# Optimization experiments

Hardware: AMD Instinct MI355X
Metric: run time of the kernel (lower is better)

Reference implementation:

```python
import jax, jax.numpy as jnp
import numpy as np

D_MODEL = 1024
NHEAD = 16
D_K = D_MODEL // NHEAD
MAX_REL = 1024


def setup_inputs() -> dict:
    key = jax.random.key(0)
    ks = jax.random.split(key, 6)
    B, S = 4, 2048
    s = 1.0 / np.sqrt(D_MODEL)
    x = jax.random.normal(ks[0], (B, S, D_MODEL), dtype=jnp.float32)
    W_qkv = jax.random.normal(ks[1], (D_MODEL, 3 * D_MODEL), dtype=jnp.float32) * s
    b_qkv = jnp.zeros((3 * D_MODEL,), dtype=jnp.float32)
    W_out = jax.random.normal(ks[2], (D_MODEL, D_MODEL), dtype=jnp.float32) * s
    b_out = jnp.zeros((D_MODEL,), dtype=jnp.float32)
    # torch init is zeros; use small random so bias path is exercised
    rel_bias = jax.random.normal(ks[3], (2 * MAX_REL + 1, NHEAD), dtype=jnp.float32) * 0.02
    return {"x": x, "W_qkv": W_qkv, "b_qkv": b_qkv, "W_out": W_out,
            "b_out": b_out, "rel_bias": rel_bias}


def reference(x, W_qkv, b_qkv, W_out, b_out, rel_bias):
    B, S, D = x.shape
    qkv = x @ W_qkv + b_qkv                      # [B,S,3D]
    qkv = qkv.reshape(B, S, 3, NHEAD, D_K)
    q, k, v = qkv[:, :, 0], qkv[:, :, 1], qkv[:, :, 2]  # [B,S,H,dk]
    # scores: [B,H,S,S]
    scores = jnp.einsum('bihd,bjhd->bhij', q, k) / jnp.sqrt(jnp.float32(D_K))
    idxs = jnp.arange(S)
    rel = jnp.clip(idxs[:, None] - idxs[None, :] + MAX_REL, 0, 2 * MAX_REL)  # [S,S]
    bias = rel_bias[rel]                         # [S,S,H]
    scores = scores + jnp.transpose(bias, (2, 0, 1))[None]  # broadcast over batch
    attn = jax.nn.softmax(scores, axis=-1)       # dropout p=0 (eval)
    out = jnp.einsum('bhij,bjhd->bihd', attn, v).reshape(B, S, D)
    return out @ W_out + b_out
```

## Files before the change

### kernel.cpp

```cpp
#include <hip/hip_runtime.h>

#define S_LEN 2048
#define NHEADS 16
#define DK 64
#define DMODEL 1024
#define QSCALE 0.18033688011f

typedef float f32x4 __attribute__((ext_vector_type(4)));
typedef _Float16 f16x8 __attribute__((ext_vector_type(8)));
typedef _Float16 f16x4 __attribute__((ext_vector_type(4)));
typedef __fp16 h16x2 __attribute__((ext_vector_type(2)));

__device__ __forceinline__ unsigned short f2h_bits(float f) {
  _Float16 h = (_Float16)f;
  unsigned short u; __builtin_memcpy(&u, &h, 2); return u;
}

__device__ __forceinline__ f32x4 mfma16(f16x8 a, f16x8 b, f32x4 c) {
  return __builtin_amdgcn_mfma_f32_16x16x32_f16(a, b, c, 0, 0, 0);
}
__device__ __forceinline__ f32x4 mfma16k16(f16x4 a, f16x4 b, f32x4 c) {
  return __builtin_amdgcn_mfma_f32_16x16x16f16(a, b, c, 0, 0, 0);
}
__device__ __forceinline__ f16x8 frag_ld(const unsigned short* p) {
  return *(const f16x8*)p;
}

#define GLD_LDS(g, l)                                                          \
  __builtin_amdgcn_global_load_lds(                                            \
      (const __attribute__((address_space(1))) void*)(g),                      \
      (__attribute__((address_space(3))) void*)(l), 16, 0, 0)

__global__ void convert_f32_f16(const float* __restrict__ in,
                                unsigned short* __restrict__ out, int n4) {
  int i = blockIdx.x * blockDim.x + threadIdx.x;
  if (i < n4) {
    f32x4 v = *(const f32x4*)(in + (size_t)i * 4);
    unsigned short o[4];
#pragma unroll
    for (int j = 0; j < 4; j++) o[j] = f2h_bits(v[j]);
    *(uint2*)(out + (size_t)i * 4) = *(const uint2*)o;
  }
}

__global__ void transpose_f32_f16(const float* __restrict__ in,
                                  unsigned short* __restrict__ out, int R, int C) {
  __shared__ unsigned short tile[32][33];
  int bx = blockIdx.x * 32, by = blockIdx.y * 32;
  int tx = threadIdx.x, ty = threadIdx.y;
  for (int i = ty; i < 32; i += 8)
    tile[i][tx] = f2h_bits(in[(size_t)(by + i) * C + bx + tx]);
  __syncthreads();
  for (int i = ty; i < 32; i += 8)
    out[(size_t)(bx + i) * R + by + tx] = tile[tx][i];
}

__launch_bounds__(256)
__global__ void gemm_bt(const unsigned short* __restrict__ A,
                        const unsigned short* __restrict__ Bt,
                        int M, int N, int K, int mode,
                        const float* __restrict__ bias,
                        float* __restrict__ out0,
                        unsigned short* __restrict__ q_o,
                        unsigned short* __restrict__ k_o,
                        unsigned short* __restrict__ v_o) {
  __shared__ __attribute__((aligned(16))) unsigned short As[128 * 32];
  __shared__ __attribute__((aligned(16))) unsigned short Bs[128 * 32];
  const int tid = threadIdx.x;
  const int w = tid >> 6, lane = tid & 63;
  const int wm = w >> 1, wn = w & 1;
  const int col = lane & 15, quad = lane >> 4;
  const int m0 = blockIdx.y * 128, n0 = blockIdx.x * 128;
  const f32x4 fzero = {0.f, 0.f, 0.f, 0.f};
  f32x4 acc[4][4];
#pragma unroll
  for (int i = 0; i < 4; i++)
#pragma unroll
    for (int j = 0; j < 4; j++) acc[i][j] = fzero;

  for (int k0 = 0; k0 < K; k0 += 32) {
    __syncthreads();
#pragma unroll
    for (int it = 0; it < 2; it++) {
      int c = it * 256 + tid;
      GLD_LDS(A + (size_t)(m0 + (c >> 2)) * K + k0 + (c & 3) * 8, &As[c * 8]);
      GLD_LDS(Bt + (size_t)(n0 + (c >> 2)) * K + k0 + (c & 3) * 8, &Bs[c * 8]);
    }
    __syncthreads();
    f16x8 af[4], bfr[4];
#pragma unroll
    for (int mi = 0; mi < 4; mi++)
      af[mi] = frag_ld(&As[(wm * 64 + mi * 16 + col) * 32 + quad * 8]);
#pragma unroll
    for (int ni = 0; ni < 4; ni++)
      bfr[ni] = frag_ld(&Bs[(wn * 64 + ni * 16 + col) * 32 + quad * 8]);
#pragma unroll
    for (int mi = 0; mi < 4; mi++)
#pragma unroll
      for (int ni = 0; ni < 4; ni++)
        acc[mi][ni] = mfma16(af[mi], bfr[ni], acc[mi][ni]);
  }

#pragma unroll
  for (int mi = 0; mi < 4; mi++) {
#pragma unroll
    for (int ni = 0; ni < 4; ni++) {
      int gm_b = m0 + wm * 64 + mi * 16 + quad * 4;
      int gn = n0 + wn * 64 + ni * 16 + col;
      float bv = bias[gn];
      if (mode == 1) {
#pragma unroll
        for (int r = 0; r < 4; r++)
          out0[(size_t)(gm_b + r) * N + gn] = acc[mi][ni][r] + bv;
      } else {
        int b = gm_b >> 11, s0 = gm_b & 2047;
        int t = gn >> 10, hd = gn & 1023;
        int h = hd >> 6, d = hd & 63;
        size_t bh = (size_t)(b * NHEADS + h);
        if (t == 2) {
          unsigned short o4[4];
#pragma unroll
          for (int r = 0; r < 4; r++) o4[r] = f2h_bits(acc[mi][ni][r] + bv);
          *(uint2*)&v_o[(bh * DK + d) * S_LEN + s0] = *(const uint2*)o4;
        } else {
          unsigned short* dst = (t == 0) ? q_o : k_o;
          float sc = (t == 0) ? QSCALE : 1.0f;
#pragma unroll
          for (int r = 0; r < 4; r++)
            dst[(bh * S_LEN + s0 + r) * DK + d] = f2h_bits((acc[mi][ni][r] + bv) * sc);
        }
      }
    }
  }
}

__launch_bounds__(256, 3)
__global__ void attn_kernel(const unsigned short* __restrict__ Q,
                            const unsigned short* __restrict__ K,
                            const unsigned short* __restrict__ Vt,
                            const float* __restrict__ rel_bias,
                            unsigned short* __restrict__ ctx) {
  __shared__ __attribute__((aligned(16))) char smem[25088];
  unsigned short* Ks = (unsigned short*)smem;
  unsigned short* Vs = (unsigned short*)(smem + 8192);
  float* brev = (float*)(smem + 16384);
  float* lred = (float*)(smem + 24832);
  float* red  = (float*)smem;

  const int tid = threadIdx.x;
  const int w = tid >> 6, lane = tid & 63;
  const int col = lane & 15, quad = lane >> 4;
  const int c7 = col & 7;
  const int bid = blockIdx.x;
  const int xcd = bid & 7, slot = bid >> 3;
  const int bh = (slot >> 5) * 8 + xcd;
  const int qt = slot & 31;
  const int h = bh & (NHEADS - 1), b = bh >> 4;
  const unsigned short* qp = Q + (size_t)bh * S_LEN * DK;
  const unsigned short* kp = K + (size_t)bh * S_LEN * DK;
  const unsigned short* vp = Vt + (size_t)bh * DK * S_LEN;
  const f32x4 fzero = {0.f, 0.f, 0.f, 0.f};

  const int tbase = 1985 - qt * 64;
#pragma unroll
  for (int it = 0; it < 9; it++) {
    int idx = it * 256 + tid;
    if (idx < 2112) {
      int rel = 3072 - (tbase + idx);
      rel = rel < 0 ? 0 : (rel > 2048 ? 2048 : rel);
      brev[idx] = rel_bias[rel * NHEADS + h] * 1.44269504089f;
    }
  }

  f16x8 qb[4][2];
#pragma unroll
  for (int qs = 0; qs < 4; qs++)
#pragma unroll
    for (int ks = 0; ks < 2; ks++)
      qb[qs][ks] = frag_ld(qp + (size_t)(qt * 64 + qs * 16 + col) * DK + ks * 32 + quad * 8);

  const int cA = tid, cB = 256 + tid;
  const int rA = cA >> 3, gA = (cA & 7) ^ (rA & 7);
  const int rB = cB >> 3, gB = (cB & 7) ^ (rB & 7);
  const unsigned short* kgA = kp + rA * DK + gA * 8;
  const unsigned short* kgB = kp + rB * DK + gB * 8;
  const unsigned short* vgA = vp + (size_t)rA * S_LEN + gA * 8;
  const unsigned short* vgB = vp + (size_t)rB * S_LEN + gB * 8;
  unsigned short* lkA = &Ks[cA * 8];
  unsigned short* lkB = &Ks[cB * 8];
  unsigned short* lvA = &Vs[cA * 8];
  unsigned short* lvB = &Vs[cB * 8];

  const float* bp = &brev[w * 16 + quad * 4 - col + 15];

  f32x4 o[4][4];
  float rsum[4];
#pragma unroll
  for (int qs = 0; qs < 4; qs++) {
#pragma unroll
    for (int ds = 0; ds < 4; ds++) o[qs][ds] = fzero;
    rsum[qs] = 0.f;
  }

  const int kaoff0 = (w * 16 + col) * 64 + (quad ^ c7) * 8;
  const int kaoff1 = (w * 16 + col) * 64 + ((4 + quad) ^ c7) * 8;
  const int vgrp = ((w * 2 + (quad >> 1)) ^ c7) * 8 + (quad & 1) * 4;

  for (int ck = 0; ck < S_LEN / 64; ck++) {
    __syncthreads();
    GLD_LDS(kgA, lkA); GLD_LDS(kgB, lkB);
    GLD_LDS(vgA, lvA); GLD_LDS(vgB, lvB);
    __syncthreads();

    f16x8 ka0 = frag_ld(&Ks[kaoff0]);
    f16x8 ka1 = frag_ld(&Ks[kaoff1]);
    f16x4 vb[4];
#pragma unroll
    for (int ds = 0; ds < 4; ds++)
      vb[ds] = *(const f16x4*)&Vs[(ds * 16 + col) * 64 + vgrp];

#pragma unroll
    for (int qs = 0; qs < 4; qs++) {
      f32x4 bias4;
#pragma unroll
      for (int r = 0; r < 4; r++) bias4[r] = bp[(3 - qs) * 16 + r];
      f32x4 sc = mfma16(ka1, qb[qs][1], mfma16(ka0, qb[qs][0], bias4));
      float p0 = __builtin_amdgcn_exp2f(sc[0]);
      float p1 = __builtin_amdgcn_exp2f(sc[1]);
      float p2 = __builtin_amdgcn_exp2f(sc[2]);
      float p3 = __builtin_amdgcn_exp2f(sc[3]);
      rsum[qs] += (p0 + p1) + (p2 + p3);
      h16x2 lo = __builtin_amdgcn_cvt_pkrtz(p0, p1);
      h16x2 hi = __builtin_amdgcn_cvt_pkrtz(p2, p3);
      f16x4 pa;
      __builtin_memcpy(&pa, &lo, 4);
      __builtin_memcpy(((char*)&pa) + 4, &hi, 4);
#pragma unroll
      for (int ds = 0; ds < 4; ds++)
        o[qs][ds] = mfma16k16(pa, vb[ds], o[qs][ds]);
    }
    kgA += 64 * DK; kgB += 64 * DK; vgA += 64; vgB += 64; bp += 64;
  }

#pragma unroll
  for (int qs = 0; qs < 4; qs++) {
    rsum[qs] += __shfl_xor(rsum[qs], 16);
    rsum[qs] += __shfl_xor(rsum[qs], 32);
  }

  __syncthreads();
  for (int ws = 3; ws >= 0; ws--) {
    if (w == ws) {
#pragma unroll
      for (int qs = 0; qs < 4; qs++) {
#pragma unroll
        for (int ds = 0; ds < 4; ds++) {
#pragma unroll
          for (int r = 0; r < 4; r++) {
            int q = qs * 16 + quad * 4 + r, d = ds * 16 + col;
            if (ws == 3) red[q * 68 + d] = o[qs][ds][r];
            else         red[q * 68 + d] += o[qs][ds][r];
          }
        }
        int ql = qs * 16 + col;
        if (ws == 3) lred[ql] = rsum[qs];
        else         lred[ql] += rsum[qs];
      }
    }
    __syncthreads();
  }

#pragma unroll
  for (int pass = 0; pass < 4; pass++) {
    int ql = w * 16 + pass * 4 + quad;
    f32x4 ov = *(const f32x4*)&red[ql * 68 + col * 4];
    float inv = 1.0f / lred[ql];
    h16x2 lo = __builtin_amdgcn_cvt_pkrtz(ov[0] * inv, ov[1] * inv);
    h16x2 hi = __builtin_amdgcn_cvt_pkrtz(ov[2] * inv, ov[3] * inv);
    uint2 pkd;
    __builtin_memcpy(&pkd.x, &lo, 4);
    __builtin_memcpy(&pkd.y, &hi, 4);
    *(uint2*)&ctx[((size_t)b * S_LEN + qt * 64 + ql) * DMODEL + h * DK + col * 4] = pkd;
  }
}

extern "C" void kernel_launch(void* const* d_in, const int* in_sizes, int n_in,
                              void* d_out, int out_size, void* d_ws, size_t ws_size,
                              hipStream_t stream) {
  (void)in_sizes; (void)n_in; (void)out_size; (void)ws_size;
  const float* x        = (const float*)d_in[0];
  const float* W_qkv    = (const float*)d_in[1];
  const float* b_qkv    = (const float*)d_in[2];
  const float* W_out    = (const float*)d_in[3];
  const float* b_out    = (const float*)d_in[4];
  const float* rel_bias = (const float*)d_in[5];
  float* out = (float*)d_out;

  char* ws = (char*)d_ws;
  unsigned short* xh     = (unsigned short*)(ws + 0);
  unsigned short* ctxh   = (unsigned short*)(ws + 0);
  unsigned short* Wqkv_t = (unsigned short*)(ws + 16777216);
  unsigned short* Wout_t = (unsigned short*)(ws + 23068672);
  unsigned short* Qb     = (unsigned short*)(ws + 25165824);
  unsigned short* Kb     = (unsigned short*)(ws + 41943040);
  unsigned short* Vtb    = (unsigned short*)(ws + 58720256);

  convert_f32_f16<<<(8192 * 1024 / 4 + 255) / 256, 256, 0, stream>>>(x, xh, 8192 * 1024 / 4);
  transpose_f32_f16<<<dim3(3072 / 32, 1024 / 32), dim3(32, 8), 0, stream>>>(W_qkv, Wqkv_t, 1024, 3072);
  transpose_f32_f16<<<dim3(1024 / 32, 1024 / 32), dim3(32, 8), 0, stream>>>(W_out, Wout_t, 1024, 1024);
  gemm_bt<<<dim3(3072 / 128, 8192 / 128), 256, 0, stream>>>(
      xh, Wqkv_t, 8192, 3072, 1024, 0, b_qkv, nullptr, Qb, Kb, Vtb);
  attn_kernel<<<4 * NHEADS * (S_LEN / 64), 256, 0, stream>>>(Qb, Kb, Vtb, rel_bias, ctxh);
  gemm_bt<<<dim3(1024 / 128, 8192 / 128), 256, 0, stream>>>(
      ctxh, Wout_t, 8192, 1024, 1024, 1, b_out, out, nullptr, nullptr, nullptr);
}
```

Measured before the change: 330.0 us.

## Load K/V fragments directly from global with register double-buffering, drop LDS staging

Replaces the per-chunk LDS staging of K and V (global_load_lds plus two barriers per chunk) with direct per-wave global loads into register fragments. Each wave now handles 32 keys per 128-key chunk, and a two-slot register double buffer prefetches the next chunk while the current one is computed. The PV product moves from the 16x16x16 to the 16x16x32 MFMA with 8-wide P fragments. The extra register pressure forces launch bounds down from 3 to 2 waves per SIMD, and K/V reuse across waves now comes from cache instead of LDS. A dead first COMPUTE macro is left in, defined and then undefined.

```diff
diff --git a/kernel.cpp b/kernel.cpp
--- a/kernel.cpp
+++ b/kernel.cpp
@@ -18,9 +18,6 @@
 
 __device__ __forceinline__ f32x4 mfma16(f16x8 a, f16x8 b, f32x4 c) {
   return __builtin_amdgcn_mfma_f32_16x16x32_f16(a, b, c, 0, 0, 0);
-}
-__device__ __forceinline__ f32x4 mfma16k16(f16x4 a, f16x4 b, f32x4 c) {
-  return __builtin_amdgcn_mfma_f32_16x16x16f16(a, b, c, 0, 0, 0);
 }
 __device__ __forceinline__ f16x8 frag_ld(const unsigned short* p) {
   return *(const f16x8*)p;
@@ -134,23 +131,20 @@
   }
 }
 
-__launch_bounds__(256, 3)
+__launch_bounds__(256, 2)
 __global__ void attn_kernel(const unsigned short* __restrict__ Q,
                             const unsigned short* __restrict__ K,
                             const unsigned short* __restrict__ Vt,
                             const float* __restrict__ rel_bias,
                             unsigned short* __restrict__ ctx) {
-  __shared__ __attribute__((aligned(16))) char smem[25088];
-  unsigned short* Ks = (unsigned short*)smem;
-  unsigned short* Vs = (unsigned short*)(smem + 8192);
-  float* brev = (float*)(smem + 16384);
-  float* lred = (float*)(smem + 24832);
+  __shared__ __attribute__((aligned(16))) char smem[17664];
+  float* brev = (float*)smem;
   float* red  = (float*)smem;
+  float* lred = (float*)(smem + 17408);
 
   const int tid = threadIdx.x;
   const int w = tid >> 6, lane = tid & 63;
   const int col = lane & 15, quad = lane >> 4;
-  const int c7 = col & 7;
   const int bid = blockIdx.x;
   const int xcd = bid & 7, slot = bid >> 3;
   const int bh = (slot >> 5) * 8 + xcd;
@@ -179,20 +173,6 @@
     for (int ks = 0; ks < 2; ks++)
       qb[qs][ks] = frag_ld(qp + (size_t)(qt * 64 + qs * 16 + col) * DK + ks * 32 + quad * 8);
 
-  const int cA = tid, cB = 256 + tid;
-  const int rA = cA >> 3, gA = (cA & 7) ^ (rA & 7);
-  const int rB = cB >> 3, gB = (cB & 7) ^ (rB & 7);
-  const unsigned short* kgA = kp + rA * DK + gA * 8;
-  const unsigned short* kgB = kp + rB * DK + gB * 8;
-  const unsigned short* vgA = vp + (size_t)rA * S_LEN + gA * 8;
-  const unsigned short* vgB = vp + (size_t)rB * S_LEN + gB * 8;
-  unsigned short* lkA = &Ks[cA * 8];
-  unsigned short* lkB = &Ks[cB * 8];
-  unsigned short* lvA = &Vs[cA * 8];
-  unsigned short* lvB = &Vs[cB * 8];
-
-  const float* bp = &brev[w * 16 + quad * 4 - col + 15];
-
   f32x4 o[4][4];
   float rsum[4];
 #pragma unroll
@@ -202,45 +182,84 @@
     rsum[qs] = 0.f;
   }
 
-  const int kaoff0 = (w * 16 + col) * 64 + (quad ^ c7) * 8;
-  const int kaoff1 = (w * 16 + col) * 64 + ((4 + quad) ^ c7) * 8;
-  const int vgrp = ((w * 2 + (quad >> 1)) ^ c7) * 8 + (quad & 1) * 4;
-
-  for (int ck = 0; ck < S_LEN / 64; ck++) {
-    __syncthreads();
-    GLD_LDS(kgA, lkA); GLD_LDS(kgB, lkB);
-    GLD_LDS(vgA, lvA); GLD_LDS(vgB, lvB);
-    __syncthreads();
-
-    f16x8 ka0 = frag_ld(&Ks[kaoff0]);
-    f16x8 ka1 = frag_ld(&Ks[kaoff1]);
-    f16x4 vb[4];
-#pragma unroll
-    for (int ds = 0; ds < 4; ds++)
-      vb[ds] = *(const f16x4*)&Vs[(ds * 16 + col) * 64 + vgrp];
-
-#pragma unroll
-    for (int qs = 0; qs < 4; qs++) {
-      f32x4 bias4;
-#pragma unroll
-      for (int r = 0; r < 4; r++) bias4[r] = bp[(3 - qs) * 16 + r];
-      f32x4 sc = mfma16(ka1, qb[qs][1], mfma16(ka0, qb[qs][0], bias4));
-      float p0 = __builtin_amdgcn_exp2f(sc[0]);
-      float p1 = __builtin_amdgcn_exp2f(sc[1]);
-      float p2 = __builtin_amdgcn_exp2f(sc[2]);
-      float p3 = __builtin_amdgcn_exp2f(sc[3]);
-      rsum[qs] += (p0 + p1) + (p2 + p3);
-      h16x2 lo = __builtin_amdgcn_cvt_pkrtz(p0, p1);
-      h16x2 hi = __builtin_amdgcn_cvt_pkrtz(p2, p3);
-      f16x4 pa;
-      __builtin_memcpy(&pa, &lo, 4);
-      __builtin_memcpy(((char*)&pa) + 4, &hi, 4);
-#pragma unroll
-      for (int ds = 0; ds < 4; ds++)
-        o[qs][ds] = mfma16k16(pa, vb[ds], o[qs][ds]);
-    }
-    kgA += 64 * DK; kgB += 64 * DK; vgA += 64; vgB += 64; bp += 64;
-  }
+  const unsigned short* kqA = kp + (size_t)(w * 32 + col) * DK + quad * 8;
+  const unsigned short* vq0 = vp + (size_t)(0 + col) * S_LEN + w * 32 + quad * 4;
+  const unsigned short* vq1 = vp + (size_t)(16 + col) * S_LEN + w * 32 + quad * 4;
+  const unsigned short* vq2 = vp + (size_t)(32 + col) * S_LEN + w * 32 + quad * 4;
+  const unsigned short* vq3 = vp + (size_t)(48 + col) * S_LEN + w * 32 + quad * 4;
+  const float* bq = brev + (w * 32 + quad * 4 - col + 63);
+
+  __syncthreads();
+
+#define LOADK(dst)                                                             \
+  dst[0][0] = frag_ld(kqA);                                                    \
+  dst[0][1] = frag_ld(kqA + 32);                                               \
+  dst[1][0] = frag_ld(kqA + 16 * DK);                                          \
+  dst[1][1] = frag_ld(kqA + 16 * DK + 32);                                     \
+  kqA += 128 * DK;
+
+#define LOADV1(dst, i, p)                                                      \
+  {                                                                            \
+    f16x4 lo_ = *(const f16x4*)(p);                                            \
+    f16x4 hi_ = *(const f16x4*)(p + 16);                                       \
+    dst[i] = __builtin_shufflevector(lo_, hi_, 0, 1, 2, 3, 4, 5, 6, 7);        \
+    p += 128;                                                                  \
+  }
+#define LOADV(dst)                                                             \
+  LOADV1(dst, 0, vq0) LOADV1(dst, 1, vq1) LOADV1(dst, 2, vq2) LOADV1(dst, 3, vq3)
+
+#define COMPUTE(ka, vb)                                                        \
+  _Pragma("unroll")                                                            \
+  for (int qs = 0; qs < 4; qs++) {                                             \
+    h16x2 pk[4];                                                               \
+    _Pragma("unroll")                                                          \
+    for (int js = 0; js < 2; js++) {                                           \
+      f32x4 bias4;                                                             \
+      _Pragma("unroll")                                                        \
+      for (int r = 0; r < 4; r++) bias4[r] = bq[(js - qs) * 16 + r];           \
+      f32x4 sc = mfma16(ka[1][1 * 0 + 1] , qb[qs][1], fzero);         \
+      (void)sc;                                                                \
+    }                                                                          \
+  }
+
+#undef COMPUTE
+#define COMPUTE(ka, vb)                                                        \
+  _Pragma("unroll")                                                            \
+  for (int qs = 0; qs < 4; qs++) {                                             \
+    h16x2 pk[4];                                                               \
+    _Pragma("unroll")                                                          \
+    for (int js = 0; js < 2; js++) {                                           \
+      f32x4 bias4;                                                             \
+      _Pragma("unroll")                                                        \
+      for (int r = 0; r < 4; r++) bias4[r] = bq[(js - qs) * 16 + r];           \
+      f32x4 sc = mfma16(ka[js][1], qb[qs][1],                                  \
+                        mfma16(ka[js][0], qb[qs][0], bias4));                  \
+      float p0 = __builtin_amdgcn_exp2f(sc[0]);                                \
+      float p1 = __builtin_amdgcn_exp2f(sc[1]);                                \
+      float p2 = __builtin_amdgcn_exp2f(sc[2]);                                \
+      float p3 = __builtin_amdgcn_exp2f(sc[3]);                                \
+      rsum[qs] += (p0 + p1) + (p2 + p3);                                       \
+      pk[js * 2]     = __builtin_amdgcn_cvt_pkrtz(p0, p1);                     \
+      pk[js * 2 + 1] = __builtin_amdgcn_cvt_pkrtz(p2, p3);                     \
+    }                                                                          \
+    f16x8 pa;                                                                  \
+    __builtin_memcpy(&pa, pk, 16);                                             \
+    _Pragma("unroll")                                                          \
+    for (int ds = 0; ds < 4; ds++)                                             \
+      o[qs][ds] = mfma16(pa, vb[ds], o[qs][ds]);                               \
+  }
+
+  f16x8 kaA[2][2], kaB[2][2], vbA[4], vbB[4];
+  LOADK(kaA) LOADV(vbA)
+  for (int ck = 0; ck < 14; ck += 2) {
+    LOADK(kaB) LOADV(vbB)
+    COMPUTE(kaA, vbA) bq += 128;
+    LOADK(kaA) LOADV(vbA)
+    COMPUTE(kaB, vbB) bq += 128;
+  }
+  LOADK(kaB) LOADV(vbB)
+  COMPUTE(kaA, vbA) bq += 128;
+  COMPUTE(kaB, vbB)
 
 #pragma unroll
   for (int qs = 0; qs < 4; qs++) {
```

Measured after the change: 401.3 us. 21.6% more time.
